# Performance work log

Measured on AMD Instinct MI355X. Metric: run time of the kernel, lower is better.

The kernel has to match this reference:

```python
import jax, jax.numpy as jnp
import numpy as np

B, T, D, E = 8, 2048, 256, 4
D_E = D // E


def setup_inputs() -> dict:
    key = jax.random.key(0)
    ks = jax.random.split(key, 12)
    s = 1.0 / np.sqrt(D)
    x = jax.random.normal(ks[0], (B, T, D), dtype=jnp.float32)
    # ensure max(seq_len) == T so the padded input matches this_batch_padlen
    seq_len = jnp.concatenate([
        jax.random.randint(ks[1], (B - 1,), T // 2, T),
        jnp.array([T]),
    ]).astype(jnp.int32)
    return {
        "x": x,
        "seq_len": seq_len,
        "wq": jax.random.uniform(ks[2], (D, D), jnp.float32, -s, s),
        "bq": jax.random.uniform(ks[3], (D,), jnp.float32, -s, s),
        "wk": jax.random.uniform(ks[4], (D, D), jnp.float32, -s, s),
        "bk": jax.random.uniform(ks[5], (D,), jnp.float32, -s, s),
        "wv": jax.random.uniform(ks[6], (D, D), jnp.float32, -s, s),
        "bv": jax.random.uniform(ks[7], (D,), jnp.float32, -s, s),
        "wo": jax.random.uniform(ks[8], (D, D), jnp.float32, -s, s),
        "bo": jax.random.uniform(ks[9], (D,), jnp.float32, -s, s),
        "theta": jnp.array([50.0], dtype=jnp.float32),
    }


def _split_heads(y):
    # faithful to torch: [B,T,D] -> permute(0,2,1) -> [B,D,T] -> reshape(B*E, T, D_E)
    return jnp.transpose(y, (0, 2, 1)).reshape(B * E, T, D_E)


def reference(x, seq_len, wq, bq, wk, bk, wv, bv, wo, bo, theta):
    Q = _split_heads(x @ wq.T + bq)          # [B*E, T, D_E]
    K = _split_heads(x @ wk.T + bk)          # [B*E, T, D_E]
    V = _split_heads(x @ wv.T + bv)          # [B*E, T, D_E]

    # padding mask: zero out query rows (and key cols) past seq_len[i]
    pos = jnp.arange(T)
    valid = (pos[None, :] < seq_len[:, None])                 # [B, T]
    mask_q = jnp.repeat(valid, E, axis=0).astype(Q.dtype)     # [B*E, T]
    Q = Q * mask_q[:, :, None]
    K = K * mask_q[:, :, None]

    scale = jnp.sqrt(jnp.float32(T))
    att = jnp.einsum('bqd,bkd->bqk', Q, K) / scale            # [B*E, T, T]

    # Gaussian positional penalty (is_punish=True)
    tpos = jnp.arange(T, dtype=jnp.float32)
    diff = tpos[None, :] - tpos[:, None]                      # j - i
    punish = jnp.exp(-(diff ** 2) / (theta[0] ** 2))          # [T, T]
    att = att * punish[None, :, :]

    att = jnp.where(att == 0.0, jnp.float32(-2e20), att)
    att = jax.nn.softmax(att, axis=2)

    ctx = jnp.einsum('bqk,bkd->bqd', att, V)                  # [B*E, T, D_E]
    # faithful inverse of _split_heads: permute(0,2,1)->reshape(B,D,T)->permute
    ctx = jnp.transpose(jnp.transpose(ctx, (0, 2, 1)).reshape(B, D, T), (0, 2, 1))
    A = ctx @ wo.T + bo
    return A + x
```

## Files before the change

kernel.cpp:

```cpp
#include <hip/hip_runtime.h>
#include <math.h>
#include <stdint.h>

#define B_SZ   8
#define T_SEQ  2048
#define DIM    256
#define NH     32
#define DE     64
#define BAND   509
#define M_ROWS (B_SZ * T_SEQ)

typedef __attribute__((ext_vector_type(8))) short short8;
typedef __attribute__((ext_vector_type(4))) float floatx4;
typedef __attribute__((ext_vector_type(4))) unsigned uintx4;
typedef unsigned short ushort_t;

__device__ __forceinline__ ushort_t f2bf(float x) {
    unsigned u = __float_as_uint(x);
    u += 0x7fffu + ((u >> 16) & 1u);
    return (ushort_t)(u >> 16);
}
__device__ __forceinline__ float bf2f(ushort_t b) {
    return __uint_as_float(((unsigned)b) << 16);
}
__device__ __forceinline__ unsigned pack2(float a, float b) {
    return (unsigned)f2bf(a) | ((unsigned)f2bf(b) << 16);
}

__device__ __forceinline__ double pd_exact(int d, float th) {
    float df  = (float)d;
    float arg = (-(df * df)) / (th * th);
    double pdd = exp((double)arg);
    if (pdd < 1.17549435082228751e-38)
        return rint(pdd * 0x1p149) * 0x1p-149;
    return (double)(float)pdd;
}

__global__ __launch_bounds__(256) void prep_kernel(
    const float* __restrict__ x,
    const float* __restrict__ wq, const float* __restrict__ wk,
    const float* __restrict__ wv, const float* __restrict__ wo,
    const float* __restrict__ theta,
    ushort_t* __restrict__ xb, ushort_t* __restrict__ wb,
    float* __restrict__ thr_g, float* __restrict__ pdf_g)
{
    const int bid = blockIdx.x, tid = threadIdx.x;
    if (bid < 2048) {
        size_t i8 = ((size_t)bid * 256 + tid) * 8;
        float4 a = *(const float4*)(x + i8);
        float4 b = *(const float4*)(x + i8 + 4);
        uint4 o;
        o.x = pack2(a.x, a.y); o.y = pack2(a.z, a.w);
        o.z = pack2(b.x, b.y); o.w = pack2(b.z, b.w);
        *(uint4*)(xb + i8) = o;
    } else if (bid < 2176) {
        size_t w8 = ((size_t)(bid - 2048) * 256 + tid) * 8;
        int which = (int)(w8 >> 16);
        const float* src = (which == 0) ? wq : (which == 1) ? wk : (which == 2) ? wv : wo;
        size_t off = w8 & 65535;
        float4 a = *(const float4*)(src + off);
        float4 b = *(const float4*)(src + off + 4);
        uint4 o;
        o.x = pack2(a.x, a.y); o.y = pack2(a.z, a.w);
        o.z = pack2(b.x, b.y); o.w = pack2(b.z, b.w);
        *(uint4*)(wb + w8) = o;
    } else {
        int i = (bid - 2176) * 256 + tid;
        float th = theta[0];
        if (i < 384) pdf_g[i] = (float)pd_exact(i, th);
        if (i < 288) {
            double pdv = pd_exact(321 + i, th);
            thr_g[i] = (pdv == 0.0) ? __builtin_inff() : (float)(0x1p-150 / pdv);
        }
    }
}

__global__ __launch_bounds__(256, 2) void proj_qkv_mfma(
    const ushort_t* __restrict__ xb, const ushort_t* __restrict__ wb,
    const float* __restrict__ bq, const float* __restrict__ bk,
    const float* __restrict__ bv, const int* __restrict__ seq_len,
    ushort_t* __restrict__ Qh, ushort_t* __restrict__ Kh, ushort_t* __restrict__ Vh)
{
    __shared__ __align__(16) ushort_t Ls[4][64][68];
    const int wave = threadIdx.x >> 6, lane = threadIdx.x & 63;
    const int quad = lane >> 4, l15 = lane & 15;
    const int task = blockIdx.x * 4 + wave;
    const int nt64 = task % 12;
    const int mstrip = task / 12;
    const int mode = nt64 >> 2;
    const int nloc_base = (nt64 & 3) * 64;
    const ushort_t* Wp = wb + (size_t)mode * 65536;
    const int m0 = mstrip * 64;
    const int bb = m0 >> 11;
    const int th0 = (m0 >> 6) & 31;
    const int sl = seq_len[bb];
    ushort_t* outp = (mode == 0) ? Qh : (mode == 1) ? Kh : Vh;
    const float* bias = (mode == 0) ? bq : (mode == 1) ? bk : bv;
    const int hh = bb * 4 + (nloc_base >> 6);
    const float oscale = (mode == 0) ? 0.022097086912079612f : 1.0f;

    short8 Bf[4][8];
    #pragma unroll
    for (int nt = 0; nt < 4; ++nt) {
        int nrow = nloc_base + nt * 16 + l15;
        #pragma unroll
        for (int ks = 0; ks < 8; ++ks)
            Bf[nt][ks] = *(const short8*)(Wp + (size_t)nrow * 256 + ks * 32 + quad * 8);
    }
    float bias4[4];
    #pragma unroll
    for (int nt = 0; nt < 4; ++nt) bias4[nt] = bias[nloc_base + nt * 16 + l15];

    short8 Acur[8];
    #pragma unroll
    for (int ks = 0; ks < 8; ++ks)
        Acur[ks] = *(const short8*)(xb + (size_t)(m0 + l15) * 256 + ks * 32 + quad * 8);

    #pragma unroll
    for (int mb = 0; mb < 4; ++mb) {
        const int mb0 = m0 + mb * 16;
        short8 Anext[8];
        if (mb < 3) {
            #pragma unroll
            for (int ks = 0; ks < 8; ++ks)
                Anext[ks] = *(const short8*)(xb + (size_t)(mb0 + 16 + l15) * 256 + ks * 32 + quad * 8);
        }
        floatx4 acc[4];
        #pragma unroll
        for (int nt = 0; nt < 4; ++nt) acc[nt] = (floatx4){0.f, 0.f, 0.f, 0.f};
        #pragma unroll
        for (int ks = 0; ks < 8; ++ks)
            #pragma unroll
            for (int nt = 0; nt < 4; ++nt)
                acc[nt] = __builtin_amdgcn_mfma_f32_16x16x32_bf16(Acur[ks], Bf[nt][ks], acc[nt], 0, 0, 0);
        #pragma unroll
        for (int nt = 0; nt < 4; ++nt) {
            float v0 = (acc[nt][0] + bias4[nt]) * oscale;
            float v1 = (acc[nt][1] + bias4[nt]) * oscale;
            float v2 = (acc[nt][2] + bias4[nt]) * oscale;
            float v3 = (acc[nt][3] + bias4[nt]) * oscale;
            uint2 pk; pk.x = pack2(v0, v1); pk.y = pack2(v2, v3);
            *(uint2*)&Ls[wave][nt * 16 + l15][mb * 16 + quad * 4] = pk;
        }
        #pragma unroll
        for (int ks = 0; ks < 8; ++ks) Acur[ks] = Anext[ks];
    }

    #pragma unroll
    for (int s = 0; s < 16; ++s) {
        int dl = s * 4 + quad;
        int e0 = l15 * 4;
        uint2 pk = *(const uint2*)&Ls[wave][dl][e0];
        int q = dl * 32 + th0;
        if (mode <= 1 && q >= sl) { pk.x = 0u; pk.y = 0u; }
        *(uint2*)(outp + (((size_t)hh * T_SEQ + q) << 6) + e0) = pk;
    }
}

__global__ __launch_bounds__(256) void vtrans_kernel(const ushort_t* __restrict__ Vh,
                                                     ushort_t* __restrict__ VTp)
{
    __shared__ ushort_t Vs[256][66];
    const int tid = threadIdx.x;
    const int h = blockIdx.x >> 3, chunk = blockIdx.x & 7;
    const ushort_t* src = Vh + ((size_t)(h * T_SEQ + chunk * 256)) * DE;
    #pragma unroll
    for (int rep = 0; rep < 8; ++rep) {
        int f = rep * 256 + tid;
        int row = f >> 3, c8 = (f & 7) * 8;
        *(uint4*)&Vs[row][c8] = *(const uint4*)(src + (size_t)row * DE + c8);
    }
    __syncthreads();
    const int w = tid >> 6, lane = tid & 63;
    const int half = lane >> 5;
    const int c32 = lane & 31;
    const int cbase = c32 * 8;
    const int blk = cbase >> 6;
    const int cin = cbase & 63;
    #pragma unroll
    for (int rr = 0; rr < 8; ++rr) {
        int e = w * 16 + rr * 2 + half;
        ushort_t tmp[8];
        #pragma unroll
        for (int t = 0; t < 8; ++t) {
            int ci = cin + t;
            int j = blk * 64 + 32 * (ci >> 5) + 4 * ((ci >> 3) & 3)
                  + 16 * ((ci >> 2) & 1) + (ci & 3);
            tmp[t] = Vs[j][e];
        }
        *(uint4*)(VTp + ((size_t)(h * DE + e)) * T_SEQ + chunk * 256 + cbase) = *(uint4*)tmp;
    }
}

__global__ __launch_bounds__(256) void meanv_partial(const ushort_t* __restrict__ Vh,
                                                     float* __restrict__ mv) {
    __shared__ float red[32][72];
    const int blk = blockIdx.x;
    const int h = blk >> 3, chunk = blk & 7;
    const int tid = threadIdx.x;
    const int r0 = tid >> 3;
    const int es = (tid & 7) * 8;
    const ushort_t* p = Vh + ((size_t)h * T_SEQ + chunk * 256 + r0) * DE + es;
    float s[8] = {};
    #pragma unroll
    for (int k = 0; k < 8; ++k) {
        uint4 u = *(const uint4*)(p + (size_t)k * 32 * DE);
        const ushort_t* w = (const ushort_t*)&u;
        #pragma unroll
        for (int i = 0; i < 8; ++i) s[i] += bf2f(w[i]);
    }
    #pragma unroll
    for (int i = 0; i < 8; ++i) red[r0][es + i] = s[i];
    __syncthreads();
    if (tid < 64) {
        float t = 0.f;
        #pragma unroll
        for (int g = 0; g < 32; ++g) t += red[g][tid];
        atomicAdd(&mv[h * DE + tid], t);
    }
}

__global__ __launch_bounds__(256) void attn_mfma_kernel(
    const ushort_t* __restrict__ Qh, const ushort_t* __restrict__ Kh,
    const ushort_t* __restrict__ VTp, const float* __restrict__ thr_g,
    const float* __restrict__ pdf_g, const float* __restrict__ mvs,
    const int* __restrict__ seq_len, ushort_t* __restrict__ ctxb)
{
    __shared__ ushort_t Ks [64][72];
    __shared__ ushort_t VTs[64][72];
    __shared__ float pdfs[384];
    __shared__ float thrs[288];

    const int tid  = threadIdx.x;
    const int wave = tid >> 6;
    const int lane = tid & 63;
    const int quad = lane >> 4;
    const int l15  = lane & 15;
    const int bid   = blockIdx.x;
    const int inner = bid >> 3;
    const int g     = inner >> 5;
    const int strip = ((inner & 31) + g * 8) & 31;
    const int h  = (g << 3) | (bid & 7);
    const int q0 = strip * 64;
    const int b  = h >> 2;
    const int sl = seq_len[b];
    const float invT = 1.0f / (float)T_SEQ;
    ushort_t* outbase = ctxb + ((size_t)b * T_SEQ + q0) * DIM + (size_t)(h & 3) * 64;

    if (q0 >= sl) {
        #pragma unroll
        for (int nt = 0; nt < 4; ++nt) {
            ushort_t mval = f2bf(mvs[h * DE + l15 + 16 * nt] * invT);
            #pragma unroll
            for (int r = 0; r < 4; ++r)
                outbase[(size_t)(wave * 16 + quad * 4 + r) * DIM + l15 + 16 * nt] = mval;
        }
        return;
    }

    for (int i = tid; i < 384; i += 256) pdfs[i] = pdf_g[i];
    for (int i = tid; i < 288; i += 256) thrs[i] = thr_g[i];

    short8 qa0, qa1;
    {
        const ushort_t* qp = Qh + ((size_t)h * T_SEQ + q0 + wave * 16 + l15) * DE + quad * 8;
        qa0 = *(const short8*)(qp);
        qa1 = *(const short8*)(qp + 32);
    }

    float l_acc = 0.f;
    floatx4 cacc[4];
    #pragma unroll
    for (int nt = 0; nt < 4; ++nt) cacc[nt] = (floatx4){0.f, 0.f, 0.f, 0.f};

    int jlo = q0 - BAND;      if (jlo < 0) jlo = 0;
    int jhi = q0 + 63 + BAND; if (jhi > sl - 1) jhi = sl - 1;
    const int jt0 = jlo >> 6, jt1 = jhi >> 6;

    const int krow = tid >> 3;
    const int kc8  = (tid & 7) * 8;
    const ushort_t* Kbp = Kh + (size_t)h * T_SEQ * DE;
    const ushort_t* Vbp = VTp + (size_t)h * DE * T_SEQ;
    uint4 kpre0, kpre1, vpre0, vpre1;
    {
        const int j0 = jt0 << 6;
        kpre0 = *(const uint4*)(Kbp + (size_t)(j0 + krow) * DE + kc8);
        kpre1 = *(const uint4*)(Kbp + (size_t)(j0 + krow + 32) * DE + kc8);
        vpre0 = *(const uint4*)(Vbp + (size_t)krow * T_SEQ + j0 + kc8);
        vpre1 = *(const uint4*)(Vbp + (size_t)(krow + 32) * T_SEQ + j0 + kc8);
    }

    const int qrow = q0 + wave * 16 + l15;

    for (int jt = jt0; jt <= jt1; ++jt) {
        const int j0 = jt << 6;
        __syncthreads();
        *(uint4*)&Ks[krow][kc8]       = kpre0;
        *(uint4*)&Ks[krow + 32][kc8]  = kpre1;
        *(uint4*)&VTs[krow][kc8]      = vpre0;
        *(uint4*)&VTs[krow + 32][kc8] = vpre1;
        __syncthreads();
        if (jt < jt1) {
            const int jn = j0 + 64;
            kpre0 = *(const uint4*)(Kbp + (size_t)(jn + krow) * DE + kc8);
            kpre1 = *(const uint4*)(Kbp + (size_t)(jn + krow + 32) * DE + kc8);
            vpre0 = *(const uint4*)(Vbp + (size_t)krow * T_SEQ + jn + kc8);
            vpre1 = *(const uint4*)(Vbp + (size_t)(krow + 32) * T_SEQ + jn + kc8);
        }

        floatx4 ST[4];
        #pragma unroll
        for (int nt = 0; nt < 4; ++nt) {
            short8 ka0 = *(const short8*)&Ks[l15 + 16 * nt][quad * 8];
            short8 ka1 = *(const short8*)&Ks[l15 + 16 * nt][32 + quad * 8];
            floatx4 z = {0.f, 0.f, 0.f, 0.f};
            z = __builtin_amdgcn_mfma_f32_16x16x32_bf16(ka0, qa0, z, 0, 0, 0);
            z = __builtin_amdgcn_mfma_f32_16x16x32_bf16(ka1, qa1, z, 0, 0, 0);
            ST[nt] = z;
        }

        const int off = j0 - q0;
        const int db  = j0 + quad * 4 - qrow;
        float p[4][4];
        if (off >= -320 && off <= 320) {
            if (j0 + 63 < sl) {
                #pragma unroll
                for (int nt = 0; nt < 4; ++nt)
                    #pragma unroll
                    for (int r = 0; r < 4; ++r) {
                        int dd = db + nt * 16 + r; dd = dd < 0 ? -dd : dd;
                        p[nt][r] = __expf(ST[nt][r] * pdfs[dd]);
                    }
            } else {
                #pragma unroll
                for (int nt = 0; nt < 4; ++nt)
                    #pragma unroll
                    for (int r = 0; r < 4; ++r) {
                        int dd = db + nt * 16 + r; dd = dd < 0 ? -dd : dd;
                        float v = __expf(ST[nt][r] * pdfs[dd]);
                        p[nt][r] = (j0 + nt * 16 + quad * 4 + r < sl) ? v : 0.f;
                    }
            }
        } else {
            #pragma unroll
            for (int nt = 0; nt < 4; ++nt)
                #pragma unroll
                for (int r = 0; r < 4; ++r) {
                    int dd = db + nt * 16 + r; dd = dd < 0 ? -dd : dd;
                    p[nt][r] = (fabsf(ST[nt][r]) > thrs[dd - 321]) ? 1.0f : 0.0f;
                }
        }

        #pragma unroll
        for (int nt = 0; nt < 4; ++nt)
            l_acc += (p[nt][0] + p[nt][1]) + (p[nt][2] + p[nt][3]);

        uintx4 t0, t1;
        t0.x = pack2(p[0][0], p[0][1]); t0.y = pack2(p[0][2], p[0][3]);
        t0.z = pack2(p[1][0], p[1][1]); t0.w = pack2(p[1][2], p[1][3]);
        t1.x = pack2(p[2][0], p[2][1]); t1.y = pack2(p[2][2], p[2][3]);
        t1.z = pack2(p[3][0], p[3][1]); t1.w = pack2(p[3][2], p[3][3]);
        short8 pa0 = __builtin_bit_cast(short8, t0);
        short8 pa1 = __builtin_bit_cast(short8, t1);

        #pragma unroll
        for (int nt = 0; nt < 4; ++nt) {
            short8 vb0 = *(const short8*)&VTs[l15 + 16 * nt][quad * 8];
            short8 vb1 = *(const short8*)&VTs[l15 + 16 * nt][32 + quad * 8];
            floatx4 c = cacc[nt];
            c = __builtin_amdgcn_mfma_f32_16x16x32_bf16(pa0, vb0, c, 0, 0, 0);
            c = __builtin_amdgcn_mfma_f32_16x16x32_bf16(pa1, vb1, c, 0, 0, 0);
            cacc[nt] = c;
        }
    }

    l_acc += __shfl_xor(l_acc, 16);
    l_acc += __shfl_xor(l_acc, 32);
    const float linv = 1.0f / l_acc;
    float linv4[4];
    #pragma unroll
    for (int r = 0; r < 4; ++r) linv4[r] = __shfl(linv, quad * 4 + r);

    #pragma unroll
    for (int nt = 0; nt < 4; ++nt) {
        #pragma unroll
        for (int r = 0; r < 4; ++r) {
            int row = wave * 16 + quad * 4 + r;
            int qg = q0 + row;
            float o = cacc[nt][r] * linv4[r];
            if (qg >= sl) o = mvs[h * DE + l15 + 16 * nt] * invT;
            outbase[(size_t)row * DIM + l15 + 16 * nt] = f2bf(o);
        }
    }
}

__global__ __launch_bounds__(256, 2) void proj_o_mfma(
    const ushort_t* __restrict__ ctx, const ushort_t* __restrict__ wb,
    const float* __restrict__ bo, const float* __restrict__ x,
    float* __restrict__ out)
{
    __shared__ __align__(16) ushort_t As[32][264];
    const int tid = threadIdx.x;
    const int wave = tid >> 6, lane = tid & 63;
    const int quad = lane >> 4, l15 = lane & 15;
    const int m0 = blockIdx.x * 32;
    const int n0 = wave * 64;
    const ushort_t* Wp = wb + (size_t)3 * 65536;

    #pragma unroll
    for (int rep = 0; rep < 4; ++rep) {
        int f = rep * 256 + tid;
        int row = f >> 5, c8 = (f & 31) * 8;
        *(uint4*)&As[row][c8] = *(const uint4*)(ctx + (size_t)(m0 + row) * 256 + c8);
    }

    short8 Bf[4][8];
    #pragma unroll
    for (int nt = 0; nt < 4; ++nt) {
        int nrow = n0 + nt * 16 + l15;
        #pragma unroll
        for (int ks = 0; ks < 8; ++ks)
            Bf[nt][ks] = *(const short8*)(Wp + (size_t)nrow * 256 + ks * 32 + quad * 8);
    }
    float bias4[4];
    #pragma unroll
    for (int nt = 0; nt < 4; ++nt) bias4[nt] = bo[n0 + nt * 16 + l15];

    __syncthreads();

    #pragma unroll
    for (int mb = 0; mb < 2; ++mb) {
        short8 Af[8];
        #pragma unroll
        for (int ks = 0; ks < 8; ++ks)
            Af[ks] = *(const short8*)&As[mb * 16 + l15][ks * 32 + quad * 8];
        floatx4 acc[4];
        #pragma unroll
        for (int nt = 0; nt < 4; ++nt) acc[nt] = (floatx4){0.f, 0.f, 0.f, 0.f};
        #pragma unroll
        for (int ks = 0; ks < 8; ++ks)
            #pragma unroll
            for (int nt = 0; nt < 4; ++nt)
                acc[nt] = __builtin_amdgcn_mfma_f32_16x16x32_bf16(Af[ks], Bf[nt][ks], acc[nt], 0, 0, 0);
        #pragma unroll
        for (int nt = 0; nt < 4; ++nt) {
            int d = n0 + nt * 16 + l15;
            #pragma unroll
            for (int r = 0; r < 4; ++r) {
                size_t mi = (size_t)(m0 + mb * 16 + quad * 4 + r) * 256 + d;
                out[mi] = acc[nt][r] + bias4[nt] + x[mi];
            }
        }
    }
}

extern "C" void kernel_launch(void* const* d_in, const int* in_sizes, int n_in,
                              void* d_out, int out_size, void* d_ws, size_t ws_size,
                              hipStream_t stream)
{
    (void)in_sizes; (void)n_in; (void)out_size; (void)ws_size;
    const float* x  = (const float*)d_in[0];
    const int*   sl = (const int*)d_in[1];
    const float* wq = (const float*)d_in[2];
    const float* bq = (const float*)d_in[3];
    const float* wk = (const float*)d_in[4];
    const float* bk = (const float*)d_in[5];
    const float* wv = (const float*)d_in[6];
    const float* bv = (const float*)d_in[7];
    const float* wo = (const float*)d_in[8];
    const float* bo = (const float*)d_in[9];
    const float* th = (const float*)d_in[10];
    float* out = (float*)d_out;

    char* ws = (char*)d_ws;
    const size_t SZH = (size_t)M_ROWS * DIM * sizeof(ushort_t);
    ushort_t* xb  = (ushort_t*)(ws);
    ushort_t* wb  = (ushort_t*)(ws + SZH);
    ushort_t* Qh  = (ushort_t*)(ws + SZH + 524288);
    ushort_t* Kh  = (ushort_t*)(ws + 2*SZH + 524288);
    ushort_t* Vh  = (ushort_t*)(ws + 3*SZH + 524288);
    ushort_t* VTp = (ushort_t*)(ws + 4*SZH + 524288);
    ushort_t* Cb  = (ushort_t*)(ws + 5*SZH + 524288);
    float*    Mv  = (float*)   (ws + 6*SZH + 524288);
    float*    Thr = (float*)   (ws + 6*SZH + 524288 + 8192);
    float*    Pdf = (float*)   (ws + 6*SZH + 524288 + 12288);

    hipMemsetAsync(Mv, 0, NH * DE * sizeof(float), stream);
    prep_kernel<<<dim3(2178), dim3(256), 0, stream>>>(x, wq, wk, wv, wo, th, xb, wb, Thr, Pdf);
    proj_qkv_mfma<<<dim3(768), dim3(256), 0, stream>>>(xb, wb, bq, bk, bv, sl, Qh, Kh, Vh);
    vtrans_kernel<<<dim3(NH * 8), dim3(256), 0, stream>>>(Vh, VTp);
    meanv_partial<<<dim3(256), dim3(256), 0, stream>>>(Vh, Mv);
    attn_mfma_kernel<<<dim3(1024), dim3(256), 0, stream>>>(Qh, Kh, VTp, Thr, Pdf, Mv, sl, Cb);
    proj_o_mfma<<<dim3(512), dim3(256), 0, stream>>>(Cb, wb, bo, x, out);
}
```

Measured before the change: 182.1 us.

## Widen attention query strips to 128 rows and stage two K/V tiles per sync

The attention kernel now uses 512-thread blocks (8 waves) covering 128 query rows, so each staged K/V tile is shared by twice as many queries. Each loop iteration stages two 64-key tiles in double-sized shared buffers, which halves the number of barriers, and one register prefetch per thread covers each tile. The pdf and threshold lookup tables grow to match the wider per-wave offset range. The cost is half as many blocks, a larger shared-memory footprint, and waves whose rows lie past seq_len still taking part in all of their block's tiles.

```diff
diff --git a/kernel.cpp b/kernel.cpp
--- a/kernel.cpp
+++ b/kernel.cpp
@@ -67,8 +67,8 @@
     } else {
         int i = (bid - 2176) * 256 + tid;
         float th = theta[0];
-        if (i < 384) pdf_g[i] = (float)pd_exact(i, th);
-        if (i < 288) {
+        if (i < 448) pdf_g[i] = (float)pd_exact(i, th);
+        if (i < 384) {
             double pdv = pd_exact(321 + i, th);
             thr_g[i] = (pdv == 0.0) ? __builtin_inff() : (float)(0x1p-150 / pdv);
         }
@@ -220,16 +220,16 @@
     }
 }
 
-__global__ __launch_bounds__(256) void attn_mfma_kernel(
+__global__ __launch_bounds__(512) void attn_mfma_kernel(
     const ushort_t* __restrict__ Qh, const ushort_t* __restrict__ Kh,
     const ushort_t* __restrict__ VTp, const float* __restrict__ thr_g,
     const float* __restrict__ pdf_g, const float* __restrict__ mvs,
     const int* __restrict__ seq_len, ushort_t* __restrict__ ctxb)
 {
-    __shared__ ushort_t Ks [64][72];
-    __shared__ ushort_t VTs[64][72];
-    __shared__ float pdfs[384];
-    __shared__ float thrs[288];
+    __shared__ ushort_t Ks [2][64][72];
+    __shared__ ushort_t VTs[2][64][72];
+    __shared__ float pdfs[448];
+    __shared__ float thrs[384];
 
     const int tid  = threadIdx.x;
     const int wave = tid >> 6;
@@ -238,10 +238,10 @@
     const int l15  = lane & 15;
     const int bid   = blockIdx.x;
     const int inner = bid >> 3;
-    const int g     = inner >> 5;
-    const int strip = ((inner & 31) + g * 8) & 31;
+    const int g     = inner >> 4;
+    const int strip = ((inner & 15) + g * 4) & 15;
     const int h  = (g << 3) | (bid & 7);
-    const int q0 = strip * 64;
+    const int q0 = strip * 128;
     const int b  = h >> 2;
     const int sl = seq_len[b];
     const float invT = 1.0f / (float)T_SEQ;
@@ -258,8 +258,8 @@
         return;
     }
 
-    for (int i = tid; i < 384; i += 256) pdfs[i] = pdf_g[i];
-    for (int i = tid; i < 288; i += 256) thrs[i] = thr_g[i];
+    for (int i = tid; i < 448; i += 512) pdfs[i] = pdf_g[i];
+    for (int i = tid; i < 384; i += 512) thrs[i] = thr_g[i];
 
     short8 qa0, qa1;
     {
@@ -273,8 +273,8 @@
     #pragma unroll
     for (int nt = 0; nt < 4; ++nt) cacc[nt] = (floatx4){0.f, 0.f, 0.f, 0.f};
 
-    int jlo = q0 - BAND;      if (jlo < 0) jlo = 0;
-    int jhi = q0 + 63 + BAND; if (jhi > sl - 1) jhi = sl - 1;
+    int jlo = q0 - BAND;       if (jlo < 0) jlo = 0;
+    int jhi = q0 + 127 + BAND; if (jhi > sl - 1) jhi = sl - 1;
     const int jt0 = jlo >> 6, jt1 = jhi >> 6;
 
     const int krow = tid >> 3;
@@ -283,47 +283,33 @@
     const ushort_t* Vbp = VTp + (size_t)h * DE * T_SEQ;
     uint4 kpre0, kpre1, vpre0, vpre1;
     {
-        const int j0 = jt0 << 6;
-        kpre0 = *(const uint4*)(Kbp + (size_t)(j0 + krow) * DE + kc8);
-        kpre1 = *(const uint4*)(Kbp + (size_t)(j0 + krow + 32) * DE + kc8);
-        vpre0 = *(const uint4*)(Vbp + (size_t)krow * T_SEQ + j0 + kc8);
-        vpre1 = *(const uint4*)(Vbp + (size_t)(krow + 32) * T_SEQ + j0 + kc8);
+        const int ja = jt0 << 6;
+        const int jb = ((jt0 + 1 <= jt1) ? jt0 + 1 : jt1) << 6;
+        kpre0 = *(const uint4*)(Kbp + (size_t)(ja + krow) * DE + kc8);
+        vpre0 = *(const uint4*)(Vbp + (size_t)krow * T_SEQ + ja + kc8);
+        kpre1 = *(const uint4*)(Kbp + (size_t)(jb + krow) * DE + kc8);
+        vpre1 = *(const uint4*)(Vbp + (size_t)krow * T_SEQ + jb + kc8);
     }
 
     const int qrow = q0 + wave * 16 + l15;
 
-    for (int jt = jt0; jt <= jt1; ++jt) {
-        const int j0 = jt << 6;
-        __syncthreads();
-        *(uint4*)&Ks[krow][kc8]       = kpre0;
-        *(uint4*)&Ks[krow + 32][kc8]  = kpre1;
-        *(uint4*)&VTs[krow][kc8]      = vpre0;
-        *(uint4*)&VTs[krow + 32][kc8] = vpre1;
-        __syncthreads();
-        if (jt < jt1) {
-            const int jn = j0 + 64;
-            kpre0 = *(const uint4*)(Kbp + (size_t)(jn + krow) * DE + kc8);
-            kpre1 = *(const uint4*)(Kbp + (size_t)(jn + krow + 32) * DE + kc8);
-            vpre0 = *(const uint4*)(Vbp + (size_t)krow * T_SEQ + jn + kc8);
-            vpre1 = *(const uint4*)(Vbp + (size_t)(krow + 32) * T_SEQ + jn + kc8);
-        }
-
+    auto subtile = [&](int s, int j0s) {
         floatx4 ST[4];
         #pragma unroll
         for (int nt = 0; nt < 4; ++nt) {
-            short8 ka0 = *(const short8*)&Ks[l15 + 16 * nt][quad * 8];
-            short8 ka1 = *(const short8*)&Ks[l15 + 16 * nt][32 + quad * 8];
+            short8 ka0 = *(const short8*)&Ks[s][l15 + 16 * nt][quad * 8];
+            short8 ka1 = *(const short8*)&Ks[s][l15 + 16 * nt][32 + quad * 8];
             floatx4 z = {0.f, 0.f, 0.f, 0.f};
             z = __builtin_amdgcn_mfma_f32_16x16x32_bf16(ka0, qa0, z, 0, 0, 0);
             z = __builtin_amdgcn_mfma_f32_16x16x32_bf16(ka1, qa1, z, 0, 0, 0);
             ST[nt] = z;
         }
 
-        const int off = j0 - q0;
-        const int db  = j0 + quad * 4 - qrow;
+        const int offw = j0s - q0 - wave * 16;
+        const int db   = j0s + quad * 4 - qrow;
         float p[4][4];
-        if (off >= -320 && off <= 320) {
-            if (j0 + 63 < sl) {
+        if (offw > -384 && offw < 336) {
+            if (j0s + 63 < sl) {
                 #pragma unroll
                 for (int nt = 0; nt < 4; ++nt)
                     #pragma unroll
@@ -338,7 +324,7 @@
                     for (int r = 0; r < 4; ++r) {
                         int dd = db + nt * 16 + r; dd = dd < 0 ? -dd : dd;
                         float v = __expf(ST[nt][r] * pdfs[dd]);
-                        p[nt][r] = (j0 + nt * 16 + quad * 4 + r < sl) ? v : 0.f;
+                        p[nt][r] = (j0s + nt * 16 + quad * 4 + r < sl) ? v : 0.f;
                     }
             }
         } else {
@@ -365,13 +351,35 @@
 
         #pragma unroll
         for (int nt = 0; nt < 4; ++nt) {
-            short8 vb0 = *(const short8*)&VTs[l15 + 16 * nt][quad * 8];
-            short8 vb1 = *(const short8*)&VTs[l15 + 16 * nt][32 + quad * 8];
+            short8 vb0 = *(const short8*)&VTs[s][l15 + 16 * nt][quad * 8];
+            short8 vb1 = *(const short8*)&VTs[s][l15 + 16 * nt][32 + quad * 8];
             floatx4 c = cacc[nt];
             c = __builtin_amdgcn_mfma_f32_16x16x32_bf16(pa0, vb0, c, 0, 0, 0);
             c = __builtin_amdgcn_mfma_f32_16x16x32_bf16(pa1, vb1, c, 0, 0, 0);
             cacc[nt] = c;
         }
+    };
+
+    for (int jt = jt0; jt <= jt1; jt += 2) {
+        const int j0a = jt << 6;
+        const bool has_b = (jt + 1 <= jt1);
+        const int j0b = (has_b ? jt + 1 : jt1) << 6;
+        __syncthreads();
+        *(uint4*)&Ks [0][krow][kc8] = kpre0;
+        *(uint4*)&VTs[0][krow][kc8] = vpre0;
+        *(uint4*)&Ks [1][krow][kc8] = kpre1;
+        *(uint4*)&VTs[1][krow][kc8] = vpre1;
+        __syncthreads();
+        if (jt + 2 <= jt1) {
+            const int jn0 = (jt + 2) << 6;
+            const int jn1 = ((jt + 3 <= jt1) ? jt + 3 : jt1) << 6;
+            kpre0 = *(const uint4*)(Kbp + (size_t)(jn0 + krow) * DE + kc8);
+            vpre0 = *(const uint4*)(Vbp + (size_t)krow * T_SEQ + jn0 + kc8);
+            kpre1 = *(const uint4*)(Kbp + (size_t)(jn1 + krow) * DE + kc8);
+            vpre1 = *(const uint4*)(Vbp + (size_t)krow * T_SEQ + jn1 + kc8);
+        }
+        subtile(0, j0a);
+        if (has_b) subtile(1, j0b);
     }
 
     l_acc += __shfl_xor(l_acc, 16);
@@ -490,6 +498,6 @@
     proj_qkv_mfma<<<dim3(768), dim3(256), 0, stream>>>(xb, wb, bq, bk, bv, sl, Qh, Kh, Vh);
     vtrans_kernel<<<dim3(NH * 8), dim3(256), 0, stream>>>(Vh, VTp);
     meanv_partial<<<dim3(256), dim3(256), 0, stream>>>(Vh, Mv);
-    attn_mfma_kernel<<<dim3(1024), dim3(256), 0, stream>>>(Qh, Kh, VTp, Thr, Pdf, Mv, sl, Cb);
+    attn_mfma_kernel<<<dim3(512), dim3(512), 0, stream>>>(Qh, Kh, VTp, Thr, Pdf, Mv, sl, Cb);
     proj_o_mfma<<<dim3(512), dim3(256), 0, stream>>>(Cb, wb, bo, x, out);
 }
```

Result: faster. 172.6 us (-5.2%).
